# Optimization experiments

Hardware: AMD Instinct MI355X
Metric: run time of the kernel (lower is better)

Reference implementation:

```python
import jax, jax.numpy as jnp
import numpy as np

NUM_HEADS = 12  # per init_kwargs


def setup_inputs() -> dict:
    key = jax.random.key(0)
    k1, k2, k3 = jax.random.split(key, 3)
    B, H, W, D = 1, 64, 64, 768
    x = jax.random.normal(k1, (B, H, W, D), dtype=jnp.float32)
    # torch nn.Linear weights are [out, in]; small init keeps softmax well-conditioned
    w_qkv = jax.random.normal(k2, (3 * D, D), dtype=jnp.float32) * 0.02
    w_proj = jax.random.normal(k3, (D, D), dtype=jnp.float32) * 0.02
    b_proj = jnp.zeros((D,), dtype=jnp.float32)
    return {"x": x, "w_qkv": w_qkv, "w_proj": w_proj, "b_proj": b_proj}


def reference(x, w_qkv, w_proj, b_proj):
    B, H, W, D = x.shape
    S = H * W
    nh = NUM_HEADS
    hd = D // nh
    scale = hd ** (-0.5)
    # qkv: [B, S, 3, nh, hd] -> q,k,v each [B, nh, S, hd]
    qkv = jnp.einsum('bhwd,ed->bhwe', x, w_qkv).reshape(B, S, 3, nh, hd)
    qkv = jnp.transpose(qkv, (2, 0, 3, 1, 4))
    q, k, v = qkv[0], qkv[1], qkv[2]
    # full O(S^2) attention matrix, as in the original module
    wei = jnp.einsum('bnqd,bnkd->bnqk', q * scale, k)
    wei = jax.nn.softmax(wei, axis=-1)
    # att_drop omitted (eval mode / deterministic baseline)
    out = jnp.einsum('bnqk,bnkd->bnqd', wei, v)  # [B, nh, S, hd]
    # [B, nh, H, W, hd] -> [B, H, W, nh*hd]
    out = jnp.transpose(out.reshape(B, nh, H, W, hd), (0, 2, 3, 1, 4)).reshape(B, H, W, D)
    proj = jnp.einsum('bhwd,ed->bhwe', out, w_proj) + b_proj
    return proj
```

## Files before the change

kernel.cpp:

```cpp
#include <hip/hip_runtime.h>
#include <hip/hip_bf16.h>
#include <math.h>

typedef short s16x8 __attribute__((ext_vector_type(8)));
typedef unsigned u32x4 __attribute__((ext_vector_type(4)));
typedef float f32x4 __attribute__((ext_vector_type(4)));
typedef float f32x16 __attribute__((ext_vector_type(16)));
typedef __hip_bfloat16 bf16;

#define GLD16(g, l)                                                        \
  __builtin_amdgcn_global_load_lds(                                        \
      (const __attribute__((address_space(1))) void*)(g),                  \
      (__attribute__((address_space(3))) void*)(l), 16, 0, 0)

#define MFMA16(a, b, c) __builtin_amdgcn_mfma_f32_16x16x32_bf16((a), (b), (c), 0, 0, 0)
#define MFMA32(a, b, c) __builtin_amdgcn_mfma_f32_32x32x16_bf16((a), (b), (c), 0, 0, 0)

static constexpr int kS = 4096;
static constexpr int kD = 768;
static constexpr int kNH = 12;
static constexpr int kHD = 64;
static constexpr int kNE = 2304;

static constexpr int kNX8 = kS * kD / 8;
static constexpr int kNWq8 = kNE * kD / 8;
static constexpr int kNWp8 = kD * kD / 8;

__global__ __launch_bounds__(256)
void k_cvt3(const float* __restrict__ x, const float* __restrict__ wq,
            const float* __restrict__ wp, bf16* __restrict__ xb,
            bf16* __restrict__ wqb, bf16* __restrict__ wpb) {
  int i = blockIdx.x * 256 + threadIdx.x;
  const float* src;
  short* dst;
  if (i < kNX8) {
    src = x; dst = (short*)xb;
  } else if (i < kNX8 + kNWq8) {
    i -= kNX8; src = wq; dst = (short*)wqb;
  } else {
    i -= kNX8 + kNWq8; if (i >= kNWp8) return;
    src = wp; dst = (short*)wpb;
  }
  const f32x4 a = *(const f32x4*)(src + i * 8);
  const f32x4 b = *(const f32x4*)(src + i * 8 + 4);
  s16x8 o;
#pragma unroll
  for (int j = 0; j < 4; ++j) {
    o[j] = (short)__bfloat16_as_ushort(__float2bfloat16(a[j]));
    o[j + 4] = (short)__bfloat16_as_ushort(__float2bfloat16(b[j]));
  }
  *(s16x8*)(dst + i * 8) = o;
}

__global__ __launch_bounds__(256, 2)
void k_qkv(const bf16* __restrict__ X, const bf16* __restrict__ W,
           bf16* __restrict__ Qw, bf16* __restrict__ Kw, bf16* __restrict__ Vw) {
  __shared__ __align__(16) short As[2][128 * 32];
  __shared__ __align__(16) short Bs[2][128 * 32];
  const int tid = threadIdx.x;
  const int wv = tid >> 6, ln = tid & 63;
  const int r = ln & 15, kq = ln >> 4;
  const int bm = blockIdx.x * 128;
  const int bn = blockIdx.y * 128;
  const int wr = wv >> 1, wc = wv & 1;
  const short* Xs = (const short*)X;
  const short* Ws = (const short*)W;

  f32x4 acc[4][4] = {};

  const int c0 = wv * 128 + ln, c1 = c0 + 64;
  const int ra0 = c0 >> 2, ka0 = c0 & 3;
  const int ra1 = c1 >> 2, ka1 = c1 & 3;
  const int off0 = wv * 1024, off1 = off0 + 512;
  const short* gA0 = Xs + (bm + ra0) * kD + ka0 * 8;
  const short* gA1 = Xs + (bm + ra1) * kD + ka1 * 8;
  const short* gB0 = Ws + (bn + ra0) * kD + ka0 * 8;
  const short* gB1 = Ws + (bn + ra1) * kD + ka1 * 8;

  GLD16(gA0, &As[0][off0]);
  GLD16(gA1, &As[0][off1]);
  GLD16(gB0, &Bs[0][off0]);
  GLD16(gB1, &Bs[0][off1]);
  __syncthreads();

  const int NT = kD / 32;
  for (int t = 0; t < NT; ++t) {
    const short* aCur = As[t & 1];
    const short* bCur = Bs[t & 1];
    if (t + 1 < NT) {
      const int k1 = (t + 1) * 32;
      short* aN = As[(t + 1) & 1];
      short* bN = Bs[(t + 1) & 1];
      GLD16(gA0 + k1, aN + off0);
      GLD16(gA1 + k1, aN + off1);
      GLD16(gB0 + k1, bN + off0);
      GLD16(gB1 + k1, bN + off1);
    }
    s16x8 a[4], b[4];
#pragma unroll
    for (int i = 0; i < 4; ++i)
      a[i] = *(const s16x8*)(aCur + (wr * 64 + i * 16 + r) * 32 + kq * 8);
#pragma unroll
    for (int j = 0; j < 4; ++j)
      b[j] = *(const s16x8*)(bCur + (wc * 64 + j * 16 + r) * 32 + kq * 8);
#pragma unroll
    for (int i = 0; i < 4; ++i)
#pragma unroll
      for (int j = 0; j < 4; ++j) acc[i][j] = MFMA16(a[i], b[j], acc[i][j]);
    __syncthreads();
  }

  const int which = bn / kD;
  bf16* dst = (which == 0) ? Qw : (which == 1) ? Kw : Vw;
  const float scl = (which == 0) ? 0.125f : 1.0f;
  const int ebase = bn - which * kD + wc * 64;
#pragma unroll
  for (int j = 0; j < 4; ++j) {
    const int e = ebase + j * 16 + r;
    const int h = e >> 6, d = e & 63;
#pragma unroll
    for (int i = 0; i < 4; ++i) {
      const int srow = bm + wr * 64 + i * 16 + kq * 4;
#pragma unroll
      for (int rr = 0; rr < 4; ++rr)
        dst[(h * kS + srow + rr) * kHD + d] = __float2bfloat16(acc[i][j][rr] * scl);
    }
  }
}

__global__ __launch_bounds__(256, 2)
void k_vt(const bf16* __restrict__ Vw, bf16* __restrict__ Vt) {
  __shared__ __align__(16) short L[64 * 72];
  const int h = blockIdx.y, st = blockIdx.x;
  const int t = threadIdx.x;
  const short* src = (const short*)Vw + (h * kS + st * 64) * kHD;
  short* dstb = (short*)Vt + h * kHD * kS;
#pragma unroll
  for (int u = 0; u < 2; ++u) {
    const int c = u * 256 + t;
    const int row = c >> 3, ch = c & 7;
    *(s16x8*)(L + row * 72 + ch * 8) = *(const s16x8*)(src + row * kHD + ch * 8);
  }
  __syncthreads();
#pragma unroll
  for (int u = 0; u < 2; ++u) {
    const int c = u * 256 + t;
    const int d = c >> 3, ch = c & 7;
    s16x8 v;
#pragma unroll
    for (int j = 0; j < 8; ++j) v[j] = L[(ch * 8 + j) * 72 + d];
    *(s16x8*)(dstb + d * kS + st * 64 + ch * 8) = v;
  }
}

__global__ __launch_bounds__(256, 3)
void k_attn(const bf16* __restrict__ Qw, const bf16* __restrict__ Kw,
            const bf16* __restrict__ Vt, bf16* __restrict__ Att) {
  __shared__ __align__(16) short Ks[3][64 * 64];
  __shared__ __align__(16) short Vs[3][64 * 64];
  const int tid = threadIdx.x;
  const int wv = tid >> 6, ln = tid & 63;
  const int qh = wv >> 1;
  const int kvh = wv & 1;
  const int col = ln & 31;
  const int lh = ln >> 5;

  const int wg = blockIdx.x;
  const int p = (wg & 7) >> 1;
  const int b = (((wg >> 3) << 1) | (wg & 1));
  const int hh = 3 * p + (b >> 6);
  const int q0 = (b & 63) * 64;

  const short* Qh = (const short*)Qw + ((size_t)hh * kS + q0 + qh * 32) * kHD;
  const short* Kh = (const short*)Kw + (size_t)hh * kS * kHD;
  const short* Vh = (const short*)Vt + (size_t)hh * kHD * kS;

  s16x8 bq[4];
#pragma unroll
  for (int kb = 0; kb < 4; ++kb)
    bq[kb] = *(const s16x8*)(Qh + col * kHD + kb * 16 + lh * 8);

  f32x16 o[2] = {};
  float lp = 0.f;

  int ldso[2];
  const short* gK[2];
  const short* gV[2];
#pragma unroll
  for (int u = 0; u < 2; ++u) {
    const int c = u * 256 + tid;
    const int kr = c >> 3, g = (c & 7) ^ (kr & 7);
    ldso[u] = c * 8;
    gK[u] = Kh + kr * kHD + g * 8;
    gV[u] = Vh + kr * kS + g * 8;
  }

#pragma unroll
  for (int u = 0; u < 2; ++u) {
    GLD16(gK[u], &Ks[0][ldso[u]]);
    GLD16(gV[u], &Vs[0][ldso[u]]);
  }
#pragma unroll
  for (int u = 0; u < 2; ++u) {
    GLD16(gK[u] + 64 * kHD, &Ks[1][ldso[u]]);
    GLD16(gV[u] + 64, &Vs[1][ldso[u]]);
  }
  asm volatile("s_waitcnt vmcnt(4)" ::: "memory");
  __builtin_amdgcn_s_barrier();

  const int NT = kS / 64;
  for (int kt = 0; kt < NT; ++kt) {
    const short* ksCur = Ks[kt % 3];
    const short* vsCur = Vs[kt % 3];
    if (kt + 2 < NT) {
      short* ksN = Ks[(kt + 2) % 3];
      short* vsN = Vs[(kt + 2) % 3];
      const int dk = (kt + 2) * 64 * kHD;
      const int dv = (kt + 2) * 64;
#pragma unroll
      for (int u = 0; u < 2; ++u) {
        GLD16(gK[u] + dk, ksN + ldso[u]);
        GLD16(gV[u] + dv, vsN + ldso[u]);
      }
    }

    f32x16 z = {};
    const int krow = kvh * 32 + col;
    const int ksw = krow & 7;
    __builtin_amdgcn_s_setprio(1);
#pragma unroll
    for (int kb = 0; kb < 4; ++kb) {
      const int ch = ((kb << 1) + lh) ^ ksw;
      s16x8 ak = *(const s16x8*)(ksCur + krow * 64 + ch * 8);
      z = MFMA32(ak, bq[kb], z);
    }
    __builtin_amdgcn_s_setprio(0);

    float pv[16];
#pragma unroll
    for (int g = 0; g < 16; ++g) {
      pv[g] = __expf(z[g]);
      lp += pv[g];
    }
    unsigned own[8], oth[8];
#pragma unroll
    for (int m = 0; m < 4; ++m) {
      own[2 * m] = (unsigned)__bfloat16_as_ushort(__float2bfloat16(pv[4 * m])) |
                   ((unsigned)__bfloat16_as_ushort(__float2bfloat16(pv[4 * m + 1])) << 16);
      own[2 * m + 1] = (unsigned)__bfloat16_as_ushort(__float2bfloat16(pv[4 * m + 2])) |
                       ((unsigned)__bfloat16_as_ushort(__float2bfloat16(pv[4 * m + 3])) << 16);
    }
#pragma unroll
    for (int i = 0; i < 8; ++i) oth[i] = __shfl_xor(own[i], 32);

    __builtin_amdgcn_s_setprio(1);
#pragma unroll
    for (int kvk = 0; kvk < 2; ++kvk) {
      u32x4 apv;
      apv[0] = lh ? oth[4 * kvk + 2] : own[4 * kvk + 0];
      apv[1] = lh ? oth[4 * kvk + 3] : own[4 * kvk + 1];
      apv[2] = lh ? own[4 * kvk + 2] : oth[4 * kvk + 0];
      apv[3] = lh ? own[4 * kvk + 3] : oth[4 * kvk + 1];
      const s16x8 ap = __builtin_bit_cast(s16x8, apv);
      const int kvg = kvh * 2 + kvk;
#pragma unroll
      for (int db = 0; db < 2; ++db) {
        const int vrow = db * 32 + col;
        const int ch = ((kvg << 1) + lh) ^ (vrow & 7);
        s16x8 vb = *(const s16x8*)(vsCur + vrow * 64 + ch * 8);
        o[db] = MFMA32(ap, vb, o[db]);
      }
    }
    __builtin_amdgcn_s_setprio(0);

    if (kt + 2 < NT)
      asm volatile("s_waitcnt vmcnt(4)" ::: "memory");
    else
      asm volatile("s_waitcnt vmcnt(0)" ::: "memory");
    __builtin_amdgcn_s_barrier();
  }

  lp += __shfl_xor(lp, 32);
  float* Of = (float*)Ks;
  float* Lf = (float*)Vs;

  if (kvh == 1) {
#pragma unroll
    for (int db = 0; db < 2; ++db)
#pragma unroll
      for (int g = 0; g < 16; ++g) {
        const int qoff = (g & 3) + 8 * (g >> 2) + 4 * lh;
        Of[(qh * 32 + qoff) * 64 + db * 32 + col] = o[db][g];
      }
    if (lh == 0) Lf[qh * 32 + col] = lp;
  }
  __syncthreads();
  if (kvh == 0) {
    lp += Lf[qh * 32 + col];
    const float inv = 1.0f / lp;
    float invq[16];
#pragma unroll
    for (int g = 0; g < 16; ++g) {
      const int qoff = (g & 3) + 8 * (g >> 2) + 4 * lh;
      invq[g] = __shfl(inv, qoff);
    }
#pragma unroll
    for (int db = 0; db < 2; ++db)
#pragma unroll
      for (int g = 0; g < 16; ++g) {
        const int qoff = (g & 3) + 8 * (g >> 2) + 4 * lh;
        const int srow = q0 + qh * 32 + qoff;
        const float val =
            (o[db][g] + Of[(qh * 32 + qoff) * 64 + db * 32 + col]) * invq[g];
        Att[srow * kD + hh * kHD + db * 32 + col] = __float2bfloat16(val);
      }
  }
}

__global__ __launch_bounds__(256, 3)
void k_proj(const bf16* __restrict__ A, const bf16* __restrict__ W,
            const float* __restrict__ Bias, float* __restrict__ Out) {
  __shared__ __align__(16) short As[2][64 * 32];
  __shared__ __align__(16) short Bs[2][64 * 32];
  const int tid = threadIdx.x;
  const int wv = tid >> 6, ln = tid & 63;
  const int r = ln & 15, kq = ln >> 4;
  const int bm = blockIdx.x * 64;
  const int bn = blockIdx.y * 64;
  const int wr = wv >> 1, wc = wv & 1;
  const short* Asrc = (const short*)A;
  const short* Wsrc = (const short*)W;

  f32x4 acc[2][2] = {};
  const int c = wv * 64 + ln;
  const int ra = c >> 2, ka = c & 3;
  const int off = wv * 512;
  const short* gA = Asrc + (bm + ra) * kD + ka * 8;
  const short* gB = Wsrc + (bn + ra) * kD + ka * 8;

  GLD16(gA, &As[0][off]);
  GLD16(gB, &Bs[0][off]);
  __syncthreads();

  const int NT = kD / 32;
  for (int t = 0; t < NT; ++t) {
    const short* aCur = As[t & 1];
    const short* bCur = Bs[t & 1];
    if (t + 1 < NT) {
      const int k1 = (t + 1) * 32;
      GLD16(gA + k1, &As[(t + 1) & 1][off]);
      GLD16(gB + k1, &Bs[(t + 1) & 1][off]);
    }
    s16x8 a[2], b[2];
#pragma unroll
    for (int i = 0; i < 2; ++i)
      a[i] = *(const s16x8*)(aCur + (wr * 32 + i * 16 + r) * 32 + kq * 8);
#pragma unroll
    for (int j = 0; j < 2; ++j)
      b[j] = *(const s16x8*)(bCur + (wc * 32 + j * 16 + r) * 32 + kq * 8);
#pragma unroll
    for (int i = 0; i < 2; ++i)
#pragma unroll
      for (int j = 0; j < 2; ++j) acc[i][j] = MFMA16(a[i], b[j], acc[i][j]);
    __syncthreads();
  }
#pragma unroll
  for (int j = 0; j < 2; ++j) {
    const int e = bn + wc * 32 + j * 16 + r;
    const float bv = Bias[e];
#pragma unroll
    for (int i = 0; i < 2; ++i) {
      const int srow = bm + wr * 32 + i * 16 + kq * 4;
#pragma unroll
      for (int rr = 0; rr < 4; ++rr)
        Out[(srow + rr) * kD + e] = acc[i][j][rr] + bv;
    }
  }
}

extern "C" void kernel_launch(void* const* d_in, const int* in_sizes, int n_in,
                              void* d_out, int out_size, void* d_ws, size_t ws_size,
                              hipStream_t stream) {
  const float* x = (const float*)d_in[0];
  const float* w_qkv = (const float*)d_in[1];
  const float* w_proj = (const float*)d_in[2];
  const float* b_proj = (const float*)d_in[3];
  float* out = (float*)d_out;

  const size_t HS = (size_t)kNH * kS * kHD;
  const int nX = kS * kD;
  const int nWq = kNE * kD;
  const int nWp = kD * kD;

  bf16* Xb = (bf16*)d_ws;
  bf16* Wqb = Xb + nX;
  bf16* Wpb = Wqb + nWq;
  bf16* Qw = Wpb + nWp;
  bf16* Kw = Qw + HS;
  bf16* Vw = Kw + HS;
  bf16* Vt = Vw + HS;
  bf16* At = Vt + HS;

  const int totalC = kNX8 + kNWq8 + kNWp8;
  k_cvt3<<<(totalC + 255) / 256, 256, 0, stream>>>(x, w_qkv, w_proj, Xb, Wqb, Wpb);

  k_qkv<<<dim3(kS / 128, kNE / 128), 256, 0, stream>>>(Xb, Wqb, Qw, Kw, Vw);
  k_vt<<<dim3(kS / 64, kNH), 256, 0, stream>>>(Vw, Vt);
  k_attn<<<dim3((kS / 64) * kNH), 256, 0, stream>>>(Qw, Kw, Vt, At);
  k_proj<<<dim3(kS / 64, kD / 64), 256, 0, stream>>>(At, Wpb, b_proj, out);
}
```

Before: 135.7 us.

## Process two KV tiles per iteration with rotating triple-buffered LDS pointers

The attention loop is unrolled by two. Both QK^T MFMA blocks are issued before either softmax/PV step, so the exp work of one tile can overlap the matrix ops of the other. Prefetch now loads two tiles at once into rotating LDS buffers, with one barrier pair per two tiles instead of per tile. The cost is more live registers for the two score accumulators and runtime pointer rotation in place of compile-time buffer indexing, which may reduce occupancy.

```diff
diff --git a/kernel.cpp b/kernel.cpp
--- a/kernel.cpp
+++ b/kernel.cpp
@@ -195,38 +195,27 @@
     gV[u] = Vh + kr * kS + g * 8;
   }
 
-#pragma unroll
-  for (int u = 0; u < 2; ++u) {
-    GLD16(gK[u], &Ks[0][ldso[u]]);
-    GLD16(gV[u], &Vs[0][ldso[u]]);
-  }
-#pragma unroll
-  for (int u = 0; u < 2; ++u) {
-    GLD16(gK[u] + 64 * kHD, &Ks[1][ldso[u]]);
-    GLD16(gV[u] + 64, &Vs[1][ldso[u]]);
+  short* ksb0 = Ks[0]; short* ksb1 = Ks[1]; short* ksb2 = Ks[2];
+  short* vsb0 = Vs[0]; short* vsb1 = Vs[1]; short* vsb2 = Vs[2];
+
+#pragma unroll
+  for (int t = 0; t < 3; ++t) {
+    short* kd = (t == 0) ? ksb0 : (t == 1) ? ksb1 : ksb2;
+    short* vd = (t == 0) ? vsb0 : (t == 1) ? vsb1 : vsb2;
+#pragma unroll
+    for (int u = 0; u < 2; ++u) {
+      GLD16(gK[u] + t * 64 * kHD, kd + ldso[u]);
+      GLD16(gV[u] + t * 64, vd + ldso[u]);
+    }
   }
   asm volatile("s_waitcnt vmcnt(4)" ::: "memory");
   __builtin_amdgcn_s_barrier();
 
-  const int NT = kS / 64;
-  for (int kt = 0; kt < NT; ++kt) {
-    const short* ksCur = Ks[kt % 3];
-    const short* vsCur = Vs[kt % 3];
-    if (kt + 2 < NT) {
-      short* ksN = Ks[(kt + 2) % 3];
-      short* vsN = Vs[(kt + 2) % 3];
-      const int dk = (kt + 2) * 64 * kHD;
-      const int dv = (kt + 2) * 64;
-#pragma unroll
-      for (int u = 0; u < 2; ++u) {
-        GLD16(gK[u] + dk, ksN + ldso[u]);
-        GLD16(gV[u] + dv, vsN + ldso[u]);
-      }
-    }
-
+  const int krow = kvh * 32 + col;
+  const int ksw = krow & 7;
+
+  auto qk = [&](const short* ksCur) -> f32x16 {
     f32x16 z = {};
-    const int krow = kvh * 32 + col;
-    const int ksw = krow & 7;
     __builtin_amdgcn_s_setprio(1);
 #pragma unroll
     for (int kb = 0; kb < 4; ++kb) {
@@ -235,7 +224,9 @@
       z = MFMA32(ak, bq[kb], z);
     }
     __builtin_amdgcn_s_setprio(0);
-
+    return z;
+  };
+  auto smpv = [&](const f32x16& z, const short* vsCur) {
     float pv[16];
 #pragma unroll
     for (int g = 0; g < 16; ++g) {
@@ -252,7 +243,6 @@
     }
 #pragma unroll
     for (int i = 0; i < 8; ++i) oth[i] = __shfl_xor(own[i], 32);
-
     __builtin_amdgcn_s_setprio(1);
 #pragma unroll
     for (int kvk = 0; kvk < 2; ++kvk) {
@@ -272,12 +262,41 @@
       }
     }
     __builtin_amdgcn_s_setprio(0);
-
-    if (kt + 2 < NT)
+  };
+
+  const int NT = kS / 64;
+  for (int kt = 0; kt < NT; kt += 2) {
+    f32x16 z0 = qk(ksb0);
+    f32x16 z1 = qk(ksb1);
+    smpv(z0, vsb0);
+    smpv(z1, vsb1);
+
+    __builtin_amdgcn_s_barrier();
+
+    if (kt + 3 < NT) {
+      const int dk = (kt + 3) * 64 * kHD, dv = (kt + 3) * 64;
+#pragma unroll
+      for (int u = 0; u < 2; ++u) {
+        GLD16(gK[u] + dk, ksb0 + ldso[u]);
+        GLD16(gV[u] + dv, vsb0 + ldso[u]);
+      }
+    }
+    if (kt + 4 < NT) {
+      const int dk = (kt + 4) * 64 * kHD, dv = (kt + 4) * 64;
+#pragma unroll
+      for (int u = 0; u < 2; ++u) {
+        GLD16(gK[u] + dk, ksb1 + ldso[u]);
+        GLD16(gV[u] + dv, vsb1 + ldso[u]);
+      }
+    }
+    if (kt + 4 < NT)
       asm volatile("s_waitcnt vmcnt(4)" ::: "memory");
     else
       asm volatile("s_waitcnt vmcnt(0)" ::: "memory");
     __builtin_amdgcn_s_barrier();
+
+    short* tk = ksb2; ksb2 = ksb1; ksb1 = ksb0; ksb0 = tk;
+    short* tv = vsb2; vsb2 = vsb1; vsb1 = vsb0; vsb0 = tv;
   }
 
   lp += __shfl_xor(lp, 32);
```

After: 134.5 us. About the same (-0.9%).
